# Optimization experiments

Measured on AMD Instinct MI355X. Metric: run time of the kernel, lower is better.

Reference implementation:

```python
import jax, jax.numpy as jnp
import numpy as np

B, C, INTER, T, H, W = 2, 256, 64, 8, 32, 32


def setup_inputs() -> dict:
    key = jax.random.key(0)
    ks = jax.random.split(key, 4)
    scale_q = 1.0 / np.sqrt(C)
    x = jax.random.normal(ks[0], (B, C, T, H, W), dtype=jnp.float32)
    Wq = jax.random.normal(ks[1], (INTER, C), dtype=jnp.float32) * scale_q
    Wk = jax.random.normal(ks[2], (INTER, C), dtype=jnp.float32) * scale_q
    Wv = jax.random.normal(ks[3], (C, C), dtype=jnp.float32) * scale_q
    return {
        "x": x,
        "Wq": Wq, "bq": jnp.zeros((INTER,), jnp.float32),
        "Wk": Wk, "bk": jnp.zeros((INTER,), jnp.float32),
        "Wv": Wv, "bv": jnp.zeros((C,), jnp.float32),
    }


def reference(x, Wq, bq, Wk, bk, Wv, bv):
    b, c, t, h, w = x.shape
    n = t * h * w
    xf = x.reshape(b, c, n)  # [B, C, N] (row-major flatten over T,H,W)
    # 1x1x1 Conv3d == per-voxel linear projection
    q = jnp.einsum('oc,bcn->bno', Wq, xf) + bq          # [B, N, INTER]
    k = jnp.einsum('oc,bcn->bon', Wk, xf) + bk[:, None]  # [B, INTER, N]
    v = jnp.einsum('oc,bcn->bon', Wv, xf) + bv[:, None]  # [B, C, N]
    energy = jnp.einsum('bid,bdj->bij', q, k)            # [B, N, N]
    attention = jax.nn.softmax(energy, axis=-1)
    # out[b,c,i] = sum_j v[b,c,j] * attention[b,i,j]
    out = jnp.einsum('bcj,bij->bci', v, attention)       # [B, C, N]
    out = out.reshape(b, c, t, h, w) + x
    return out
```

## Files before the change

kernel.cpp:

```cpp
#include <hip/hip_runtime.h>
#include <hip/hip_bf16.h>

typedef short short8 __attribute__((ext_vector_type(8)));
typedef float float4v __attribute__((ext_vector_type(4)));

#define MFMA(a, b, c) __builtin_amdgcn_mfma_f32_16x16x32_bf16((a), (b), (c), 0, 0, 0)

typedef const __attribute__((address_space(1))) unsigned int gu32;
typedef __attribute__((address_space(3))) unsigned int lu32;
#define GLOAD_LDS16(g, l) __builtin_amdgcn_global_load_lds((gu32*)(g), (lu32*)(l), 16, 0, 0)

#define LOG2E 1.4426950408889634f

static __device__ __forceinline__ unsigned short f2bf(float f) {
    union { float f; unsigned u; } v; v.f = f;
    unsigned r = (v.u + 0x7fffu + ((v.u >> 16) & 1u)) >> 16;
    return (unsigned short)r;
}
static __device__ __forceinline__ float bf2f(unsigned short h) {
    union { unsigned u; float f; } v; v.u = ((unsigned)h) << 16;
    return v.f;
}
static __device__ __forceinline__ unsigned pk2bf(float a, float b) {
    union { __hip_bfloat162 h; unsigned u; } cv;
    cv.h = __float22bfloat162_rn(make_float2(a, b));
    return cv.u;
}

static __device__ __forceinline__ int qk_idx(int b, int n, int o) {
    int frag = (b * 512 + (n >> 4)) * 2 + (o >> 5);
    return frag * 512 + ((o >> 3) & 3) * 128 + (n & 15) * 8 + (o & 7);
}
static __device__ __forceinline__ int v_idx(int b, int c, int n) {
    int frag = (b * 256 + (n >> 5)) * 16 + (c >> 4);
    return frag * 512 + ((n >> 3) & 3) * 128 + (c & 15) * 8 + (n & 7);
}

__global__ void wcvt(const float* __restrict__ Wq, const float* __restrict__ Wk,
                     const float* __restrict__ Wv,
                     unsigned short* __restrict__ Whi, unsigned short* __restrict__ Wlo) {
    int idx = blockIdx.x * 256 + threadIdx.x;
    if (idx >= 384 * 256) return;
    int row = idx >> 8, c = idx & 255;
    float f;
    if (row < 64)       f = Wq[row * 256 + c];
    else if (row < 128) f = Wk[(row - 64) * 256 + c];
    else                f = Wv[(row - 128) * 256 + c];
    unsigned short hi = f2bf(f);
    Whi[idx] = hi;
    if (row < 128) Wlo[idx] = f2bf(f - bf2f(hi));
}

__global__ __launch_bounds__(256, 1) void proj(
        const float* __restrict__ x, const unsigned short* __restrict__ Whi,
        const unsigned short* __restrict__ Wlo,
        const float* __restrict__ bq, const float* __restrict__ bk,
        const float* __restrict__ bv,
        unsigned short* __restrict__ qhi_ws, unsigned short* __restrict__ qlo_ws,
        unsigned short* __restrict__ khi_ws, unsigned short* __restrict__ klo_ws,
        unsigned short* __restrict__ vws) {
    __shared__ unsigned short XThi[64 * 264];
    __shared__ unsigned short XTlo[64 * 264];

    const int tid = threadIdx.x;
    const int b  = blockIdx.x >> 7;
    const int n0 = (blockIdx.x & 127) << 6;
    const float* xb = x + b * 2097152;

    for (int p = 0; p < 16; ++p) {
        int idx = p * 256 + tid;
        int c = idx >> 4, nq = idx & 15;
        float4v xv = *reinterpret_cast<const float4v*>(xb + c * 8192 + n0 + nq * 4);
#pragma unroll
        for (int q = 0; q < 4; ++q) {
            unsigned short hi = f2bf(xv[q]);
            XThi[(nq * 4 + q) * 264 + c] = hi;
            XTlo[(nq * 4 + q) * 264 + c] = f2bf(xv[q] - bf2f(hi));
        }
    }
    __syncthreads();

    const int lane = tid & 63, w = tid >> 6;
    const int quad = lane >> 4, l16 = lane & 15;

    short8 aXhi[8], aXlo[8];
#pragma unroll
    for (int ks = 0; ks < 8; ++ks) {
        aXhi[ks] = *reinterpret_cast<const short8*>(&XThi[(w * 16 + l16) * 264 + ks * 32 + quad * 8]);
        aXlo[ks] = *reinterpret_cast<const short8*>(&XTlo[(w * 16 + l16) * 264 + ks * 32 + quad * 8]);
    }

#pragma unroll
    for (int ot = 0; ot < 8; ++ot) {
        float4v acc = {0.f, 0.f, 0.f, 0.f};
#pragma unroll
        for (int ks = 0; ks < 8; ++ks) {
            short8 bwhi = *reinterpret_cast<const short8*>(&Whi[(ot * 16 + l16) * 256 + ks * 32 + quad * 8]);
            short8 bwlo = *reinterpret_cast<const short8*>(&Wlo[(ot * 16 + l16) * 256 + ks * 32 + quad * 8]);
            acc = MFMA(aXhi[ks], bwhi, acc);
            acc = MFMA(aXlo[ks], bwhi, acc);
            acc = MFMA(aXhi[ks], bwlo, acc);
        }
        int o = ot * 16 + l16;
        float bias = (ot < 4) ? bq[o] : bk[o - 64];
#pragma unroll
        for (int r = 0; r < 4; ++r) {
            int n = n0 + w * 16 + quad * 4 + r;
            float y = acc[r] + bias;
            if (ot < 4) y *= LOG2E;
            unsigned short hi = f2bf(y);
            unsigned short lo = f2bf(y - bf2f(hi));
            if (ot < 4) {
                int id = qk_idx(b, n, o);
                qhi_ws[id] = hi; qlo_ws[id] = lo;
            } else {
                int id = qk_idx(b, n, o - 64);
                khi_ws[id] = hi; klo_ws[id] = lo;
            }
        }
    }

    float4v acc2[4][4];
#pragma unroll
    for (int mt = 0; mt < 4; ++mt)
#pragma unroll
        for (int nt = 0; nt < 4; ++nt) acc2[mt][nt] = (float4v){0.f, 0.f, 0.f, 0.f};

#pragma unroll
    for (int ks = 0; ks < 8; ++ks) {
        short8 aW[4], bX[4];
#pragma unroll
        for (int mt = 0; mt < 4; ++mt)
            aW[mt] = *reinterpret_cast<const short8*>(&Whi[(128 + w * 64 + mt * 16 + l16) * 256 + ks * 32 + quad * 8]);
#pragma unroll
        for (int nt = 0; nt < 4; ++nt)
            bX[nt] = *reinterpret_cast<const short8*>(&XThi[(nt * 16 + l16) * 264 + ks * 32 + quad * 8]);
#pragma unroll
        for (int mt = 0; mt < 4; ++mt)
#pragma unroll
            for (int nt = 0; nt < 4; ++nt)
                acc2[mt][nt] = MFMA(aW[mt], bX[nt], acc2[mt][nt]);
    }
#pragma unroll
    for (int mt = 0; mt < 4; ++mt) {
#pragma unroll
        for (int r = 0; r < 4; ++r) {
            int c = w * 64 + mt * 16 + quad * 4 + r;
            float bias = bv[c];
#pragma unroll
            for (int nt = 0; nt < 4; ++nt) {
                int n = n0 + nt * 16 + l16;
                vws[v_idx(b, c, n)] = f2bf(acc2[mt][nt][r] + bias);
            }
        }
    }
}

__global__ __launch_bounds__(256, 2) void attn(
        const unsigned short* __restrict__ qhi_ws, const unsigned short* __restrict__ qlo_ws,
        const unsigned short* __restrict__ khi_ws, const unsigned short* __restrict__ klo_ws,
        const unsigned short* __restrict__ vws,
        unsigned short* __restrict__ Opart, float* __restrict__ ml) {
    __shared__ unsigned short Vlds[3][8192];
    __shared__ unsigned short Klds[2][4096];
    __shared__ unsigned short Pl[4 * 32 * 36];

    const int tid = threadIdx.x, lane = tid & 63, w = tid >> 6;
    const int quad = lane >> 4, l16 = lane & 15;
    const int xcd = blockIdx.x & 7, b = xcd & 1, jr = xcd >> 1;
    const int it = blockIdx.x >> 3;
    const int iw16 = it * 8 + w * 2;
    unsigned short* Pw = Pl + w * (32 * 36);

    const unsigned short* qhb = qhi_ws + (size_t)((b * 512 + iw16) * 2) * 512 + lane * 8;
    const unsigned short* qlb = qlo_ws + (size_t)((b * 512 + iw16) * 2) * 512 + lane * 8;
    short8 qh[2][2], ql[2][2];
#pragma unroll
    for (int mt = 0; mt < 2; ++mt)
#pragma unroll
        for (int kf = 0; kf < 2; ++kf) {
            qh[mt][kf] = *reinterpret_cast<const short8*>(qhb + (mt * 2 + kf) * 512);
            ql[mt][kf] = *reinterpret_cast<const short8*>(qlb + (mt * 2 + kf) * 512);
        }

    const unsigned short* khs = khi_ws + (size_t)((b * 512 + jr * 128) * 2) * 512 + w * 512 + lane * 8;
    const unsigned short* kls = klo_ws + (size_t)((b * 512 + jr * 128) * 2) * 512 + w * 512 + lane * 8;
    const unsigned short* vstage = vws + ((size_t)(b * 256 + jr * 64) * 16 + w * 4) * 512 + lane * 8;

    float4v acc[2][16];
#pragma unroll
    for (int mt = 0; mt < 2; ++mt)
#pragma unroll
        for (int cf = 0; cf < 16; ++cf) acc[mt][cf] = (float4v){0.f, 0.f, 0.f, 0.f};
    float lrow[2][4];
    short8 aP[2];
#pragma unroll
    for (int mt = 0; mt < 2; ++mt)
#pragma unroll
        for (int r = 0; r < 4; ++r) lrow[mt][r] = 0.f;

    GLOAD_LDS16(khs, &Klds[0][w * 512]);
    GLOAD_LDS16(kls, &Klds[0][2048 + w * 512]);
#pragma unroll
    for (int q = 0; q < 4; ++q)
        GLOAD_LDS16(vstage + q * 512, &Vlds[0][(w * 4 + q) * 512]);
    khs += 2048; kls += 2048; vstage += 8192;
    __syncthreads();

    int bprev = 2, bcur = 0, bnext = 1;
#pragma unroll 1
    for (int itn = 0; itn < 64; ++itn) {
        if (itn) __syncthreads();

        if (itn < 63) {
            GLOAD_LDS16(khs, &Klds[(itn + 1) & 1][w * 512]);
            GLOAD_LDS16(kls, &Klds[(itn + 1) & 1][2048 + w * 512]);
#pragma unroll
            for (int q = 0; q < 4; ++q)
                GLOAD_LDS16(vstage + q * 512, &Vlds[bnext][(w * 4 + q) * 512]);
            khs += 2048; kls += 2048; vstage += 8192;
        }

        const unsigned short* Kc = &Klds[itn & 1][0];
        float4v s[2][2];
#pragma unroll
        for (int mt = 0; mt < 2; ++mt)
#pragma unroll
            for (int jt = 0; jt < 2; ++jt) s[mt][jt] = (float4v){0.f, 0.f, 0.f, 0.f};
#pragma unroll
        for (int jt = 0; jt < 2; ++jt) {
            short8 kh0 = *reinterpret_cast<const short8*>(Kc + (jt * 2 + 0) * 512 + lane * 8);
            short8 kh1 = *reinterpret_cast<const short8*>(Kc + (jt * 2 + 1) * 512 + lane * 8);
            short8 kl0 = *reinterpret_cast<const short8*>(Kc + 2048 + (jt * 2 + 0) * 512 + lane * 8);
            short8 kl1 = *reinterpret_cast<const short8*>(Kc + 2048 + (jt * 2 + 1) * 512 + lane * 8);
#pragma unroll
            for (int mt = 0; mt < 2; ++mt) {
                s[mt][jt] = MFMA(qh[mt][0], kh0, s[mt][jt]);
                s[mt][jt] = MFMA(ql[mt][0], kh0, s[mt][jt]);
                s[mt][jt] = MFMA(qh[mt][0], kl0, s[mt][jt]);
                s[mt][jt] = MFMA(qh[mt][1], kh1, s[mt][jt]);
                s[mt][jt] = MFMA(ql[mt][1], kh1, s[mt][jt]);
                s[mt][jt] = MFMA(qh[mt][1], kl1, s[mt][jt]);
            }
        }

        if (itn) {
            const unsigned short* vl = &Vlds[bprev][0];
#pragma unroll
            for (int cf = 0; cf < 16; ++cf) {
                short8 v0 = *reinterpret_cast<const short8*>(vl + cf * 512 + lane * 8);
                acc[0][cf] = MFMA(aP[0], v0, acc[0][cf]);
                acc[1][cf] = MFMA(aP[1], v0, acc[1][cf]);
            }
        }

#pragma unroll
        for (int mt = 0; mt < 2; ++mt)
#pragma unroll
            for (int jt = 0; jt < 2; ++jt) {
                float p0 = exp2f(s[mt][jt][0]);
                float p1 = exp2f(s[mt][jt][1]);
                float p2 = exp2f(s[mt][jt][2]);
                float p3 = exp2f(s[mt][jt][3]);
                lrow[mt][0] += p0; lrow[mt][1] += p1;
                lrow[mt][2] += p2; lrow[mt][3] += p3;
                unsigned u01 = pk2bf(p0, p1);
                unsigned u23 = pk2bf(p2, p3);
                int base = (mt * 16 + quad * 4) * 36 + jt * 16 + l16;
                Pw[base]          = (unsigned short)u01;
                Pw[base + 36]     = (unsigned short)(u01 >> 16);
                Pw[base + 72]     = (unsigned short)u23;
                Pw[base + 108]    = (unsigned short)(u23 >> 16);
            }

#pragma unroll
        for (int mt = 0; mt < 2; ++mt)
            aP[mt] = *reinterpret_cast<const short8*>(&Pw[(mt * 16 + l16) * 36 + quad * 8]);

        int t = bprev; bprev = bcur; bcur = bnext; bnext = t;
    }

    {
        const unsigned short* vl = &Vlds[bprev][0];
#pragma unroll
        for (int cf = 0; cf < 16; ++cf) {
            short8 v0 = *reinterpret_cast<const short8*>(vl + cf * 512 + lane * 8);
            acc[0][cf] = MFMA(aP[0], v0, acc[0][cf]);
            acc[1][cf] = MFMA(aP[1], v0, acc[1][cf]);
        }
    }

#pragma unroll
    for (int mt = 0; mt < 2; ++mt)
#pragma unroll
        for (int r = 0; r < 4; ++r) {
            float lv = lrow[mt][r];
            lv += __shfl_xor(lv, 1);
            lv += __shfl_xor(lv, 2);
            lv += __shfl_xor(lv, 4);
            lv += __shfl_xor(lv, 8);
            if (l16 == 0) {
                int iloc = w * 32 + mt * 16 + quad * 4 + r;
                ml[blockIdx.x * 128 + iloc] = lv;
            }
        }

    unsigned short* ob = Opart + (size_t)blockIdx.x * 32768;
#pragma unroll
    for (int mt = 0; mt < 2; ++mt)
#pragma unroll
        for (int cf = 0; cf < 16; ++cf) {
            unsigned u01 = pk2bf(acc[mt][cf][0], acc[mt][cf][1]);
            unsigned u23 = pk2bf(acc[mt][cf][2], acc[mt][cf][3]);
            int iloc = w * 32 + mt * 16 + quad * 4;
            ob[(iloc + 0) * 256 + cf * 16 + l16] = (unsigned short)u01;
            ob[(iloc + 1) * 256 + cf * 16 + l16] = (unsigned short)(u01 >> 16);
            ob[(iloc + 2) * 256 + cf * 16 + l16] = (unsigned short)u23;
            ob[(iloc + 3) * 256 + cf * 16 + l16] = (unsigned short)(u23 >> 16);
        }
}

__global__ __launch_bounds__(256) void combine(
        const unsigned short* __restrict__ Opart, const float* __restrict__ ml,
        const float* __restrict__ x, float* __restrict__ out) {
    __shared__ float fac[128];
    __shared__ float trans[64 * 130];

    const int t = threadIdx.x;
    const int blk = blockIdx.x;
    const int b = blk & 1, cc = (blk >> 1) & 3, it = blk >> 3;

    if (t < 128) {
        float sum = 0.f;
#pragma unroll
        for (int s = 0; s < 4; ++s)
            sum += ml[(size_t)((it << 3) | (s << 1) | b) * 128 + t];
        fac[t] = 1.0f / sum;
    }
    __syncthreads();

    {
        const int cgrp = t & 7, irow = t >> 3;
#pragma unroll
        for (int ip = 0; ip < 4; ++ip) {
            int i = ip * 32 + irow;
            float a[8];
#pragma unroll
            for (int e = 0; e < 8; ++e) a[e] = 0.f;
#pragma unroll
            for (int s = 0; s < 4; ++s) {
                const unsigned short* op = Opart +
                    (size_t)((it << 3) | (s << 1) | b) * 32768 + i * 256 + cc * 64 + cgrp * 8;
                short8 o = *reinterpret_cast<const short8*>(op);
#pragma unroll
                for (int e = 0; e < 8; ++e) a[e] += bf2f((unsigned short)o[e]);
            }
            float f = fac[i];
#pragma unroll
            for (int e = 0; e < 8; ++e) trans[(cgrp * 8 + e) * 130 + i] = a[e] * f;
        }
    }
    __syncthreads();

    {
        const int c2 = t >> 2, iq = t & 3;
        const int cg = cc * 64 + c2;
        const float* xr = x + (size_t)b * 2097152 + (size_t)cg * 8192 + it * 128;
        float* orow = out + (size_t)b * 2097152 + (size_t)cg * 8192 + it * 128;
#pragma unroll 2
        for (int k = 0; k < 8; ++k) {
            int i = iq * 4 + k * 16;
            float4v o;
#pragma unroll
            for (int r = 0; r < 4; ++r) o[r] = trans[c2 * 130 + i + r];
            float4v xv = *reinterpret_cast<const float4v*>(xr + i);
#pragma unroll
            for (int r = 0; r < 4; ++r) o[r] += xv[r];
            *reinterpret_cast<float4v*>(orow + i) = o;
        }
    }
}

extern "C" void kernel_launch(void* const* d_in, const int* in_sizes, int n_in,
                              void* d_out, int out_size, void* d_ws, size_t ws_size,
                              hipStream_t stream) {
    const float* x  = (const float*)d_in[0];
    const float* Wq = (const float*)d_in[1];
    const float* bq = (const float*)d_in[2];
    const float* Wk = (const float*)d_in[3];
    const float* bk = (const float*)d_in[4];
    const float* Wv = (const float*)d_in[5];
    const float* bv = (const float*)d_in[6];

    unsigned short* Whi = (unsigned short*)d_ws;
    unsigned short* Wlo = Whi + 384 * 256;
    unsigned short* qhi = Wlo + 128 * 256;
    unsigned short* qlo = qhi + 2 * 8192 * 64;
    unsigned short* khi = qlo + 2 * 8192 * 64;
    unsigned short* klo = khi + 2 * 8192 * 64;
    unsigned short* vws = klo + 2 * 8192 * 64;
    unsigned short* Opart = vws + 2 * 256 * 8192;
    float* ml = (float*)(Opart + (size_t)512 * 32768);

    wcvt<<<384, 256, 0, stream>>>(Wq, Wk, Wv, Whi, Wlo);
    proj<<<256, 256, 0, stream>>>(x, Whi, Wlo, bq, bk, bv, qhi, qlo, khi, klo, vws);
    attn<<<512, 256, 0, stream>>>(qhi, qlo, khi, klo, vws, Opart, ml);
    combine<<<512, 256, 0, stream>>>(Opart, ml, x, (float*)d_out);
}
```

Baseline: 246.7 us.

## Triple-buffer K tiles with partial vmcnt waits, raise MFMA priority, unpad P buffer

Moves K staging to a three-slot ring prefetched two iterations ahead. The full __syncthreads is replaced by a partial s_waitcnt vmcnt plus a raw s_barrier, so the next tiles' global->LDS loads can stay in flight across the barrier. It also wraps the MFMA blocks in s_setprio to favour matrix issue, and removes the 36-element padding on the P scratch buffer. The risks are LDS bank conflicts from the unpadded P layout and correctness depending on the hand-counted vmcnt values matching the issued loads.

```diff
diff --git a/kernel.cpp b/kernel.cpp
--- a/kernel.cpp
+++ b/kernel.cpp
@@ -9,6 +9,8 @@
 typedef const __attribute__((address_space(1))) unsigned int gu32;
 typedef __attribute__((address_space(3))) unsigned int lu32;
 #define GLOAD_LDS16(g, l) __builtin_amdgcn_global_load_lds((gu32*)(g), (lu32*)(l), 16, 0, 0)
+
+#define VMWAIT(n) asm volatile("s_waitcnt vmcnt(" n ")" ::: "memory")
 
 #define LOG2E 1.4426950408889634f
 
@@ -162,15 +164,15 @@
         const unsigned short* __restrict__ vws,
         unsigned short* __restrict__ Opart, float* __restrict__ ml) {
     __shared__ unsigned short Vlds[3][8192];
-    __shared__ unsigned short Klds[2][4096];
-    __shared__ unsigned short Pl[4 * 32 * 36];
+    __shared__ unsigned short Klds[3][4096];
+    __shared__ unsigned short Pl[4 * 32 * 32];
 
     const int tid = threadIdx.x, lane = tid & 63, w = tid >> 6;
     const int quad = lane >> 4, l16 = lane & 15;
     const int xcd = blockIdx.x & 7, b = xcd & 1, jr = xcd >> 1;
     const int it = blockIdx.x >> 3;
     const int iw16 = it * 8 + w * 2;
-    unsigned short* Pw = Pl + w * (32 * 36);
+    unsigned short* Pw = Pl + w * (32 * 32);
 
     const unsigned short* qhb = qhi_ws + (size_t)((b * 512 + iw16) * 2) * 512 + lane * 8;
     const unsigned short* qlb = qlo_ws + (size_t)((b * 512 + iw16) * 2) * 512 + lane * 8;
@@ -204,29 +206,38 @@
 #pragma unroll
     for (int q = 0; q < 4; ++q)
         GLOAD_LDS16(vstage + q * 512, &Vlds[0][(w * 4 + q) * 512]);
-    khs += 2048; kls += 2048; vstage += 8192;
-    __syncthreads();
+    GLOAD_LDS16(khs + 2048, &Klds[1][w * 512]);
+    GLOAD_LDS16(kls + 2048, &Klds[1][2048 + w * 512]);
+    khs += 4096; kls += 4096; vstage += 8192;
 
     int bprev = 2, bcur = 0, bnext = 1;
+    int kc = 0, kst = 2;
 #pragma unroll 1
     for (int itn = 0; itn < 64; ++itn) {
-        if (itn) __syncthreads();
+        if (itn < 63) VMWAIT("6");
+        else          VMWAIT("4");
+        __builtin_amdgcn_s_barrier();
+        __builtin_amdgcn_sched_barrier(0);
 
         if (itn < 63) {
-            GLOAD_LDS16(khs, &Klds[(itn + 1) & 1][w * 512]);
-            GLOAD_LDS16(kls, &Klds[(itn + 1) & 1][2048 + w * 512]);
 #pragma unroll
             for (int q = 0; q < 4; ++q)
                 GLOAD_LDS16(vstage + q * 512, &Vlds[bnext][(w * 4 + q) * 512]);
-            khs += 2048; kls += 2048; vstage += 8192;
-        }
-
-        const unsigned short* Kc = &Klds[itn & 1][0];
+            vstage += 8192;
+        }
+        if (itn < 62) {
+            GLOAD_LDS16(khs, &Klds[kst][w * 512]);
+            GLOAD_LDS16(kls, &Klds[kst][2048 + w * 512]);
+            khs += 2048; kls += 2048;
+        }
+
+        const unsigned short* Kc = &Klds[kc][0];
         float4v s[2][2];
 #pragma unroll
         for (int mt = 0; mt < 2; ++mt)
 #pragma unroll
             for (int jt = 0; jt < 2; ++jt) s[mt][jt] = (float4v){0.f, 0.f, 0.f, 0.f};
+        __builtin_amdgcn_s_setprio(1);
 #pragma unroll
         for (int jt = 0; jt < 2; ++jt) {
             short8 kh0 = *reinterpret_cast<const short8*>(Kc + (jt * 2 + 0) * 512 + lane * 8);
@@ -243,15 +254,18 @@
                 s[mt][jt] = MFMA(qh[mt][1], kl1, s[mt][jt]);
             }
         }
+        __builtin_amdgcn_s_setprio(0);
 
         if (itn) {
             const unsigned short* vl = &Vlds[bprev][0];
+            __builtin_amdgcn_s_setprio(1);
 #pragma unroll
             for (int cf = 0; cf < 16; ++cf) {
                 short8 v0 = *reinterpret_cast<const short8*>(vl + cf * 512 + lane * 8);
                 acc[0][cf] = MFMA(aP[0], v0, acc[0][cf]);
                 acc[1][cf] = MFMA(aP[1], v0, acc[1][cf]);
             }
+            __builtin_amdgcn_s_setprio(0);
         }
 
 #pragma unroll
@@ -266,20 +280,25 @@
                 lrow[mt][2] += p2; lrow[mt][3] += p3;
                 unsigned u01 = pk2bf(p0, p1);
                 unsigned u23 = pk2bf(p2, p3);
-                int base = (mt * 16 + quad * 4) * 36 + jt * 16 + l16;
-                Pw[base]          = (unsigned short)u01;
-                Pw[base + 36]     = (unsigned short)(u01 >> 16);
-                Pw[base + 72]     = (unsigned short)u23;
-                Pw[base + 108]    = (unsigned short)(u23 >> 16);
+                int base = (mt * 16 + quad * 4) * 32 + jt * 16 + l16;
+                Pw[base]       = (unsigned short)u01;
+                Pw[base + 32]  = (unsigned short)(u01 >> 16);
+                Pw[base + 64]  = (unsigned short)u23;
+                Pw[base + 96]  = (unsigned short)(u23 >> 16);
             }
 
 #pragma unroll
         for (int mt = 0; mt < 2; ++mt)
-            aP[mt] = *reinterpret_cast<const short8*>(&Pw[(mt * 16 + l16) * 36 + quad * 8]);
+            aP[mt] = *reinterpret_cast<const short8*>(&Pw[(mt * 16 + l16) * 32 + quad * 8]);
 
         int t = bprev; bprev = bcur; bcur = bnext; bnext = t;
-    }
-
+        kc  = (kc  == 2) ? 0 : kc + 1;
+        kst = (kst == 2) ? 0 : kst + 1;
+    }
+
+    VMWAIT("0");
+    __builtin_amdgcn_s_barrier();
+    __builtin_amdgcn_sched_barrier(0);
     {
         const unsigned short* vl = &Vlds[bprev][0];
 #pragma unroll
```

After: 234.2 us. 1.05x faster.
